# Performance work log

Hardware: AMD Instinct MI355X
Metric: run time of the kernel (lower is better)

## Reference

```python
import jax, jax.numpy as jnp
import numpy as np

M1 = jnp.array([[1.0, 1.0, 1.0],
                [0.3963377774, -0.1055613458, -0.0894841775],
                [0.2158037573, -0.0638541728, -1.291485548]], dtype=jnp.float32)
M2 = jnp.array([[4.0767416621, -1.2684380046, 0.0041960863],
                [-3.3077115913, 2.6097574011, -0.7034186147],
                [0.2309699292, -0.3413193965, 1.707614701]], dtype=jnp.float32)
M3 = jnp.array([[0.613130111351449, 0.0701050973342151, 0.0205851228833001],
                [0.339523761133735, 0.916356903394254, 0.109559786350199],
                [0.0474050234857193, 0.0134571284251877, 0.869782709459968]], dtype=jnp.float32)


def setup_inputs() -> dict:
    key = jax.random.key(0)
    img = jax.random.normal(key, (8, 3, 1024, 1024), dtype=jnp.float32)
    return {"img": img}


def reference(img) -> jnp.ndarray:
    # img: [B, 3, H, W] -> per-pixel rows of 3: [B, H, W, 3]
    x = jnp.transpose(img, (0, 2, 3, 1))
    x = x @ M1                              # row-vector matmul, same as torch
    x = jnp.sign(x) * jnp.abs(x) ** 3       # signed cube
    x = (x @ M2) @ M3
    return jnp.transpose(x, (0, 3, 1, 2))   # back to [B, 3, H, W]
```

## Files before the change

### kernel.cpp

```cpp
#include <hip/hip_runtime.h>


#define B_DIM 8
#define HW (1024 * 1024)
#define QP (HW / 4)
#define NQUADS (B_DIM * QP)

__device__ __forceinline__ void oklab_px(float L, float A, float Bv,
                                         float& r, float& g, float& b) {
    float y0 = fmaf(0.2158037573f,  Bv, fmaf(0.3963377774f,  A, L));
    float y1 = fmaf(-0.0638541728f, Bv, fmaf(-0.1055613458f, A, L));
    float y2 = fmaf(-1.291485548f,  Bv, fmaf(-0.0894841775f, A, L));

    float l = y0 * y0 * y0;
    float m = y1 * y1 * y1;
    float s = y2 * y2 * y2;

    float z0 = fmaf(0.2309699292f, s, fmaf(-3.3077115913f, m, 4.0767416621f  * l));
    float z1 = fmaf(-0.3413193965f, s, fmaf(2.6097574011f,  m, -1.2684380046f * l));
    float z2 = fmaf(1.707614701f,  s, fmaf(-0.7034186147f, m, 0.0041960863f  * l));

    r = fmaf(0.0474050234857193f, z2, fmaf(0.339523761133735f,  z1, 0.613130111351449f  * z0));
    g = fmaf(0.0134571284251877f, z2, fmaf(0.916356903394254f,  z1, 0.0701050973342151f * z0));
    b = fmaf(0.869782709459968f,  z2, fmaf(0.109559786350199f,  z1, 0.0205851228833001f * z0));
}

__global__ __launch_bounds__(256) void oklab_to_acescg_kernel(
    const float4* __restrict__ in, float4* __restrict__ out) {
    int idx = blockIdx.x * blockDim.x + threadIdx.x;
    int stride = gridDim.x * blockDim.x;
    for (int t = idx; t < NQUADS; t += stride) {
        int b = t >> 18;
        int q = t & (QP - 1);
        const float4 xL = in[(b * 3 + 0) * QP + q];
        const float4 xA = in[(b * 3 + 1) * QP + q];
        const float4 xB = in[(b * 3 + 2) * QP + q];

        float4 oR, oG, oB;
        oklab_px(xL.x, xA.x, xB.x, oR.x, oG.x, oB.x);
        oklab_px(xL.y, xA.y, xB.y, oR.y, oG.y, oB.y);
        oklab_px(xL.z, xA.z, xB.z, oR.z, oG.z, oB.z);
        oklab_px(xL.w, xA.w, xB.w, oR.w, oG.w, oB.w);

        out[(b * 3 + 0) * QP + q] = oR;
        out[(b * 3 + 1) * QP + q] = oG;
        out[(b * 3 + 2) * QP + q] = oB;
    }
}

extern "C" void kernel_launch(void* const* d_in, const int* in_sizes, int n_in,
                              void* d_out, int out_size, void* d_ws, size_t ws_size,
                              hipStream_t stream) {
    const float4* in = (const float4*)d_in[0];
    float4* out = (float4*)d_out;
    int threads = 256;
    int blocks = 2048;
    oklab_to_acescg_kernel<<<blocks, threads, 0, stream>>>(in, out);
}
```

Baseline: 35.81 us.

## Replace grid-stride loop with two quads per thread and nontemporal stores

Drops the grid-stride loop and launches enough blocks that each thread handles exactly two quads, half the domain apart. All six 16-byte loads are issued up front to raise memory-level parallelism. Outputs are written with nontemporal stores to reduce cache pollution on a purely streaming write. The grid grows to 4096 blocks, which adds block scheduling overhead but removes loop control.

```diff
diff --git a/kernel.cpp b/kernel.cpp
--- a/kernel.cpp
+++ b/kernel.cpp
@@ -1,13 +1,16 @@
 #include <hip/hip_runtime.h>
 
 
-#define B_DIM 8
 #define HW (1024 * 1024)
 #define QP (HW / 4)
-#define NQUADS (B_DIM * QP)
+#define NQUADS (8 * QP)
+#define NTHREADS (NQUADS / 2)
 
-__device__ __forceinline__ void oklab_px(float L, float A, float Bv,
-                                         float& r, float& g, float& b) {
+typedef float f4 __attribute__((ext_vector_type(4)));
+
+struct Px { float r, g, b; };
+
+__device__ __forceinline__ Px oklab_px(float L, float A, float Bv) {
     float y0 = fmaf(0.2158037573f,  Bv, fmaf(0.3963377774f,  A, L));
     float y1 = fmaf(-0.0638541728f, Bv, fmaf(-0.1055613458f, A, L));
     float y2 = fmaf(-1.291485548f,  Bv, fmaf(-0.0894841775f, A, L));
@@ -20,40 +23,57 @@
     float z1 = fmaf(-0.3413193965f, s, fmaf(2.6097574011f,  m, -1.2684380046f * l));
     float z2 = fmaf(1.707614701f,  s, fmaf(-0.7034186147f, m, 0.0041960863f  * l));
 
-    r = fmaf(0.0474050234857193f, z2, fmaf(0.339523761133735f,  z1, 0.613130111351449f  * z0));
-    g = fmaf(0.0134571284251877f, z2, fmaf(0.916356903394254f,  z1, 0.0701050973342151f * z0));
-    b = fmaf(0.869782709459968f,  z2, fmaf(0.109559786350199f,  z1, 0.0205851228833001f * z0));
+    Px p;
+    p.r = fmaf(0.0474050234857193f, z2, fmaf(0.339523761133735f,  z1, 0.613130111351449f  * z0));
+    p.g = fmaf(0.0134571284251877f, z2, fmaf(0.916356903394254f,  z1, 0.0701050973342151f * z0));
+    p.b = fmaf(0.869782709459968f,  z2, fmaf(0.109559786350199f,  z1, 0.0205851228833001f * z0));
+    return p;
+}
+
+__device__ __forceinline__ void do_quad(f4 xL, f4 xA, f4 xB,
+                                        f4& oR, f4& oG, f4& oB) {
+    Px p0 = oklab_px(xL.x, xA.x, xB.x);
+    Px p1 = oklab_px(xL.y, xA.y, xB.y);
+    Px p2 = oklab_px(xL.z, xA.z, xB.z);
+    Px p3 = oklab_px(xL.w, xA.w, xB.w);
+    oR.x = p0.r; oR.y = p1.r; oR.z = p2.r; oR.w = p3.r;
+    oG.x = p0.g; oG.y = p1.g; oG.z = p2.g; oG.w = p3.g;
+    oB.x = p0.b; oB.y = p1.b; oB.z = p2.b; oB.w = p3.b;
 }
 
 __global__ __launch_bounds__(256) void oklab_to_acescg_kernel(
-    const float4* __restrict__ in, float4* __restrict__ out) {
-    int idx = blockIdx.x * blockDim.x + threadIdx.x;
-    int stride = gridDim.x * blockDim.x;
-    for (int t = idx; t < NQUADS; t += stride) {
-        int b = t >> 18;
-        int q = t & (QP - 1);
-        const float4 xL = in[(b * 3 + 0) * QP + q];
-        const float4 xA = in[(b * 3 + 1) * QP + q];
-        const float4 xB = in[(b * 3 + 2) * QP + q];
+    const f4* __restrict__ in, f4* __restrict__ out) {
+    int t0 = blockIdx.x * blockDim.x + threadIdx.x;
+    int t1 = t0 + NTHREADS;
 
-        float4 oR, oG, oB;
-        oklab_px(xL.x, xA.x, xB.x, oR.x, oG.x, oB.x);
-        oklab_px(xL.y, xA.y, xB.y, oR.y, oG.y, oB.y);
-        oklab_px(xL.z, xA.z, xB.z, oR.z, oG.z, oB.z);
-        oklab_px(xL.w, xA.w, xB.w, oR.w, oG.w, oB.w);
+    int b0 = t0 >> 18, q0 = t0 & (QP - 1);
+    int b1 = t1 >> 18, q1 = t1 & (QP - 1);
 
-        out[(b * 3 + 0) * QP + q] = oR;
-        out[(b * 3 + 1) * QP + q] = oG;
-        out[(b * 3 + 2) * QP + q] = oB;
-    }
+    const f4 aL = in[(b0 * 3 + 0) * QP + q0];
+    const f4 aA = in[(b0 * 3 + 1) * QP + q0];
+    const f4 aB = in[(b0 * 3 + 2) * QP + q0];
+    const f4 cL = in[(b1 * 3 + 0) * QP + q1];
+    const f4 cA = in[(b1 * 3 + 1) * QP + q1];
+    const f4 cB = in[(b1 * 3 + 2) * QP + q1];
+
+    f4 aR, aG, aBo, cR, cG, cBo;
+    do_quad(aL, aA, aB, aR, aG, aBo);
+    do_quad(cL, cA, cB, cR, cG, cBo);
+
+    __builtin_nontemporal_store(aR,  &out[(b0 * 3 + 0) * QP + q0]);
+    __builtin_nontemporal_store(aG,  &out[(b0 * 3 + 1) * QP + q0]);
+    __builtin_nontemporal_store(aBo, &out[(b0 * 3 + 2) * QP + q0]);
+    __builtin_nontemporal_store(cR,  &out[(b1 * 3 + 0) * QP + q1]);
+    __builtin_nontemporal_store(cG,  &out[(b1 * 3 + 1) * QP + q1]);
+    __builtin_nontemporal_store(cBo, &out[(b1 * 3 + 2) * QP + q1]);
 }
 
 extern "C" void kernel_launch(void* const* d_in, const int* in_sizes, int n_in,
                               void* d_out, int out_size, void* d_ws, size_t ws_size,
                               hipStream_t stream) {
-    const float4* in = (const float4*)d_in[0];
-    float4* out = (float4*)d_out;
+    const f4* in = (const f4*)d_in[0];
+    f4* out = (f4*)d_out;
     int threads = 256;
-    int blocks = 2048;
+    int blocks = NTHREADS / threads;
     oklab_to_acescg_kernel<<<blocks, threads, 0, stream>>>(in, out);
 }
```

Result: no change. 35.71 us (-0.3%).
